# Kernel optimization log

Hardware: AMD Instinct MI355X
Metric: run time of the kernel (lower is better)

Reference implementation:

```python
import jax, jax.numpy as jnp
import numpy as np

N, T, V, C, H = 16, 512, 33, 3, 64
EPS = 1e-5
CONNECTIONS = [(0,1),(1,2),(2,3),(3,7),(0,4),(4,5),(5,6),(6,8),(9,10),(11,12),(11,13),(13,15),(12,14),(14,16),(15,17),(15,19),(15,21),(17,19),(16,18),(16,20),(16,22),(18,20),(11,23),(12,24),(23,24),(23,25),(25,27),(24,26),(26,28),(27,29),(27,31),(29,31),(28,30),(28,32)]


def _adjacency():
    A = np.zeros((V, V), dtype=np.float32)
    for i, j in CONNECTIONS:
        A[i, j] = 1.0
        A[j, i] = 1.0
    A = A + np.eye(V, dtype=np.float32)
    return jnp.asarray(A / A.sum(axis=1, keepdims=True))  # D^{-1} A row-normalization


def setup_inputs() -> dict:
    key = jax.random.key(0)
    ks = iter(jax.random.split(key, 80))
    def nrm(shape, s=0.05):
        return jax.random.normal(next(ks), shape, jnp.float32) * s
    d = {"x": jax.random.normal(next(ks), (N, T, V, C), jnp.float32), "A": _adjacency()}
    def bn(prefix, shape):
        d[prefix + "g"] = 1.0 + nrm(shape, 0.1)
        d[prefix + "b"] = nrm(shape, 0.1)
        d[prefix + "m"] = jnp.zeros(shape, jnp.float32)
        d[prefix + "v"] = jnp.ones(shape, jnp.float32)
    bn("dbn_", (C * V,))
    d["b1_gw"] = nrm((H, C)); d["b1_gb"] = nrm((H,))
    bn("b1_bn1", (H,)); d["b1_tw"] = nrm((H, H, 9)); d["b1_tb"] = nrm((H,)); bn("b1_bn2", (H,))
    d["m_gw"] = nrm((3, H, H)); d["m_gb"] = nrm((3, H))
    bn("m_bn1", (3, H)); d["m_tw"] = nrm((3, H, H, 9)); d["m_tb"] = nrm((3, H)); bn("m_bn2", (3, H))
    d["b5_gw"] = nrm((C, H)); d["b5_gb"] = nrm((C,))
    bn("b5_bn1", (C,)); d["b5_tw"] = nrm((C, C, 9)); d["b5_tb"] = nrm((C,)); bn("b5_bn2", (C,))
    return d


def _bn2d(y, g, b, m, v):
    sh = (1, -1, 1, 1)
    return (y - m.reshape(sh)) * (g.reshape(sh) * jax.lax.rsqrt(v.reshape(sh) + EPS)) + b.reshape(sh)


def _block(y, A, gw, gb, g1, b1, m1, v1, tw, tb, g2, b2, m2, v2, residual):
    res = y if residual else 0.0
    # GraphConv: 1x1 conv (K=1 partition) then joint aggregation with normalized adjacency
    z = jnp.einsum('nctv,oc->notv', y, gw) + gb.reshape(1, -1, 1, 1)
    z = jnp.einsum('nctv,vw->nctw', z, A)
    # TCN: BN -> ReLU -> 9x1 temporal conv (pad 4) -> BN (dropout identity in eval)
    z = jax.nn.relu(_bn2d(z, g1, b1, m1, v1))
    z = jax.lax.conv_general_dilated(z, tw[..., None], (1, 1), [(4, 4), (0, 0)],
                                     dimension_numbers=('NCHW', 'OIHW', 'NCHW')) + tb.reshape(1, -1, 1, 1)
    z = _bn2d(z, g2, b2, m2, v2)
    return jax.nn.relu(z + res)


def _forward(x, A, dbn_g, dbn_b, dbn_m, dbn_v, b1_gw, b1_gb, b1_bn1g, b1_bn1b, b1_bn1m, b1_bn1v, b1_tw, b1_tb, b1_bn2g, b1_bn2b, b1_bn2m, b1_bn2v, m_gw, m_gb, m_bn1g, m_bn1b, m_bn1m, m_bn1v, m_tw, m_tb, m_bn2g, m_bn2b, m_bn2m, m_bn2v, b5_gw, b5_gb, b5_bn1g, b5_bn1b, b5_bn1m, b5_bn1v, b5_tw, b5_tb, b5_bn2g, b5_bn2b, b5_bn2m, b5_bn2v):
    xc = jnp.transpose(x, (0, 3, 1, 2))  # N,C,T,V
    # data_bn: raw view of NCTV contiguous buffer as (N, C*V, T), matching torch .view
    xr = xc.reshape(N, C * V, T)
    xr = (xr - dbn_m[:, None]) * (dbn_g[:, None] * jax.lax.rsqrt(dbn_v[:, None] + EPS)) + dbn_b[:, None]
    y = xr.reshape(N, C, T, V)
    y = _block(y, A, b1_gw, b1_gb, b1_bn1g, b1_bn1b, b1_bn1m, b1_bn1v, b1_tw, b1_tb, b1_bn2g, b1_bn2b, b1_bn2m, b1_bn2v, False)
    for i in range(3):
        y = _block(y, A, m_gw[i], m_gb[i], m_bn1g[i], m_bn1b[i], m_bn1m[i], m_bn1v[i], m_tw[i], m_tb[i], m_bn2g[i], m_bn2b[i], m_bn2m[i], m_bn2v[i], True)
    y = _block(y, A, b5_gw, b5_gb, b5_bn1g, b5_bn1b, b5_bn1m, b5_bn1v, b5_tw, b5_tb, b5_bn2g, b5_bn2b, b5_bn2m, b5_bn2v, False)
    return jnp.transpose(xc + y, (0, 2, 3, 1))  # N,T,V,C


def reference(x, A, dbn_g, dbn_b, dbn_m, dbn_v, b1_gw, b1_gb, b1_bn1g, b1_bn1b, b1_bn1m, b1_bn1v, b1_tw, b1_tb, b1_bn2g, b1_bn2b, b1_bn2m, b1_bn2v, m_gw, m_gb, m_bn1g, m_bn1b, m_bn1m, m_bn1v, m_tw, m_tb, m_bn2g, m_bn2b, m_bn2m, m_bn2v, b5_gw, b5_gb, b5_bn1g, b5_bn1b, b5_bn1m, b5_bn1v, b5_tw, b5_tb, b5_bn2g, b5_bn2b, b5_bn2m, b5_bn2v):
    return _forward(x, A, dbn_g, dbn_b, dbn_m, dbn_v, b1_gw, b1_gb, b1_bn1g, b1_bn1b, b1_bn1m, b1_bn1v, b1_tw, b1_tb, b1_bn2g, b1_bn2b, b1_bn2m, b1_bn2v, m_gw, m_gb, m_bn1g, m_bn1b, m_bn1m, m_bn1v, m_tw, m_tb, m_bn2g, m_bn2b, m_bn2m, m_bn2v, b5_gw, b5_gb, b5_bn1g, b5_bn1b, b5_bn1m, b5_bn1v, b5_tw, b5_tb, b5_bn2g, b5_bn2b, b5_bn2m, b5_bn2v)
```

## Files before the change

### kernel.cpp

```cpp
#include <hip/hip_runtime.h>
#include <hip/hip_bf16.h>


constexpr int N_ = 16, T_ = 512, V_ = 33, C_ = 3, H_ = 64;
constexpr float EPS_ = 1e-5f;

typedef __attribute__((ext_vector_type(8))) short short8;
typedef __attribute__((ext_vector_type(4))) float f32x4;

__device__ inline unsigned short f2bf(float f) {
    union { __hip_bfloat16 h; unsigned short u; } cv;
    cv.h = __float2bfloat16(f);
    return cv.u;
}
__device__ inline float bf2f(unsigned short u) {
    union { unsigned short u; __hip_bfloat16 h; } cv;
    cv.u = u;
    return __bfloat162float(cv.h);
}

__global__ __launch_bounds__(256) void k_prep(
    const float* __restrict__ b1_tw, const float* __restrict__ m_tw,
    const float* __restrict__ b1_gw, const float* __restrict__ m_gw,
    const float* __restrict__ Adj,
    unsigned short* __restrict__ wT_bf, unsigned short* __restrict__ gw_bf,
    unsigned short* __restrict__ ATbf, float* __restrict__ colsum,
    float* __restrict__ gwT_b1)
{
    int idx = blockIdx.x * 256 + threadIdx.x;
    if (idx < 147456) {
        int s = idx / 36864, r = idx % 36864;
        int k = r / 4096, o = (r % 4096) / 64, i = r % 64;
        const float* src = (s == 0) ? b1_tw : (m_tw + (size_t)(s - 1) * 36864);
        wT_bf[idx] = f2bf(src[(o * 64 + i) * 9 + k]);
    } else if (idx < 147456 + 12288) {
        int r = idx - 147456;
        gw_bf[r] = f2bf(m_gw[r]);
    } else if (idx < 147456 + 12288 + 3456) {
        int r = idx - 159744;
        int w = r / 72, vv = r % 72;
        ATbf[r] = (w < 33 && vv < 33) ? f2bf(Adj[vv * 33 + w]) : (unsigned short)0;
    } else if (idx < 147456 + 12288 + 3456 + 48) {
        int w = idx - 163200;
        float s = 0.f;
        if (w < 33)
            for (int vv = 0; vv < 33; ++vv) s += Adj[vv * 33 + w];
        colsum[w] = s;
    } else if (idx < 147456 + 12288 + 3456 + 48 + 192) {
        int r = idx - 163248;
        int c = r / 64, o = r % 64;
        gwT_b1[r] = b1_gw[o * 3 + c];
    }
}

__global__ __launch_bounds__(256) void k_stageA_b1(
    const float* __restrict__ x,
    unsigned short* __restrict__ out,
    const unsigned short* __restrict__ ATbf,
    const float* __restrict__ colsum,
    const float* __restrict__ gwT,
    const float* __restrict__ gb,
    const float* __restrict__ g1, const float* __restrict__ b1,
    const float* __restrict__ m1, const float* __restrict__ v1,
    const float* __restrict__ dg, const float* __restrict__ db,
    const float* __restrict__ dm, const float* __restrict__ dv)
{
    __shared__ float sy[4][V_ * 4];
    __shared__ unsigned short UT[64 * 72];
    __shared__ float cs[48];

    int nt0 = blockIdx.x * 4;
    int tid = threadIdx.x;
    int wv = tid >> 6, lane = tid & 63;
    int l15 = lane & 15, lg = lane >> 4;
    int o = wv * 16 + l15;

    short8 atf[3][2];
#pragma unroll
    for (int mf = 0; mf < 3; ++mf)
#pragma unroll
        for (int kk = 0; kk < 2; ++kk)
            atf[mf][kk] = *reinterpret_cast<const short8*>(
                ATbf + (16 * mf + l15) * 72 + kk * 32 + lg * 8);

    float gw0 = gwT[0 * 64 + o], gw1 = gwT[1 * 64 + o], gw2 = gwT[2 * 64 + o];
    float gbl = gb[o];
    float s1 = g1[o] * rsqrtf(v1[o] + EPS_);
    float c1 = b1[o] - m1[o] * s1;

    for (int idx = tid; idx < 4 * V_ * 3; idx += 256) {
        int j = idx / (V_ * 3), r = idx % (V_ * 3);
        int v = r / 3, c = r % 3;
        int nt = nt0 + j;
        int t = nt & (T_ - 1);
        int jj = c * V_ + ((t * V_ + v) >> 9);
        float s = dg[jj] * rsqrtf(dv[jj] + EPS_);
        sy[j][v * 4 + c] = (x[(size_t)nt * (V_ * 3) + r] - dm[jj]) * s + db[jj];
    }
    for (int idx = tid; idx < 128; idx += 256) {
        int oo = idx >> 1, cc = idx & 1;
        short8 z = {};
        *reinterpret_cast<short8*>(&UT[oo * 72 + 48 + cc * 8]) = z;
    }
    if (tid < 48) cs[tid] = colsum[tid];
    __syncthreads();

    for (int j = 0; j < 4; ++j) {
#pragma unroll
        for (int it = 0; it < 12; ++it) {
            int v = lg + it * 4;
            float u = 0.f;
            if (v < V_) {
                u = sy[j][v * 4 + 0] * gw0;
                u = fmaf(sy[j][v * 4 + 1], gw1, u);
                u = fmaf(sy[j][v * 4 + 2], gw2, u);
            }
            UT[o * 72 + v] = f2bf(u);
        }
        short8 bu[2];
#pragma unroll
        for (int kk = 0; kk < 2; ++kk)
            bu[kk] = *reinterpret_cast<const short8*>(&UT[o * 72 + kk * 32 + lg * 8]);
#pragma unroll
        for (int mf2 = 0; mf2 < 3; ++mf2) {
            f32x4 az = {};
#pragma unroll
            for (int kk = 0; kk < 2; ++kk)
                az = __builtin_amdgcn_mfma_f32_16x16x32_bf16(atf[mf2][kk], bu[kk], az, 0, 0, 0);
#pragma unroll
            for (int r = 0; r < 4; ++r) {
                int w = 16 * mf2 + lg * 4 + r;
                if (w < 33) {
                    float val = az[r] + gbl * cs[w];
                    float y = fmaxf(val * s1 + c1, 0.f);
                    out[((size_t)(nt0 + j) * V_ + w) * 64 + o] = f2bf(y);
                }
            }
        }
    }
}

__global__ __launch_bounds__(256) void k_stageA_mfma(
    const unsigned short* __restrict__ in,
    unsigned short* __restrict__ out,
    const unsigned short* __restrict__ ATbf,
    const float* __restrict__ colsum,
    const unsigned short* __restrict__ gwbf,
    const float* __restrict__ gb,
    const float* __restrict__ g1, const float* __restrict__ b1,
    const float* __restrict__ m1, const float* __restrict__ v1)
{
    __shared__ unsigned short Ys[4 * 48 * 72];
    __shared__ unsigned short UT[64 * 72];
    __shared__ float cs[48];

    int nt0 = blockIdx.x * 4;
    int tid = threadIdx.x;
    int wv = tid >> 6, lane = tid & 63;
    int l15 = lane & 15, lg = lane >> 4;
    int o = wv * 16 + l15;

    short8 atf[3][2];
#pragma unroll
    for (int mf = 0; mf < 3; ++mf)
#pragma unroll
        for (int kk = 0; kk < 2; ++kk)
            atf[mf][kk] = *reinterpret_cast<const short8*>(
                ATbf + (16 * mf + l15) * 72 + kk * 32 + lg * 8);
    short8 gwf[2];
#pragma unroll
    for (int kk = 0; kk < 2; ++kk)
        gwf[kk] = *reinterpret_cast<const short8*>(gwbf + o * 64 + kk * 32 + lg * 8);

    float gbl = gb[o];
    float s1 = g1[o] * rsqrtf(v1[o] + EPS_);
    float c1 = b1[o] - m1[o] * s1;

    for (int idx = tid; idx < 1056; idx += 256) {
        int j = idx / 264, r = idx % 264;
        int v = r >> 3, cc = r & 7;
        *reinterpret_cast<short8*>(&Ys[(j * 48 + v) * 72 + cc * 8]) =
            *reinterpret_cast<const short8*>(in + ((size_t)(nt0 + j) * V_ + v) * 64 + cc * 8);
    }
    for (int idx = tid; idx < 540; idx += 256) {
        int j = idx / 135, r = idx % 135;
        int v = 33 + r / 9, cc = r % 9;
        short8 z = {};
        *reinterpret_cast<short8*>(&Ys[(j * 48 + v) * 72 + cc * 8]) = z;
    }
    for (int idx = tid; idx < 128; idx += 256) {
        int oo = idx >> 1, cc = idx & 1;
        short8 z = {};
        *reinterpret_cast<short8*>(&UT[oo * 72 + 48 + cc * 8]) = z;
    }
    if (tid < 48) cs[tid] = colsum[tid];
    __syncthreads();

    for (int j = 0; j < 4; ++j) {
#pragma unroll
        for (int mf = 0; mf < 3; ++mf) {
            f32x4 au = {};
#pragma unroll
            for (int kk = 0; kk < 2; ++kk) {
                short8 a = *reinterpret_cast<const short8*>(
                    &Ys[(j * 48 + 16 * mf + l15) * 72 + kk * 32 + lg * 8]);
                au = __builtin_amdgcn_mfma_f32_16x16x32_bf16(a, gwf[kk], au, 0, 0, 0);
            }
            unsigned short pk[4];
            pk[0] = f2bf(au[0]); pk[1] = f2bf(au[1]);
            pk[2] = f2bf(au[2]); pk[3] = f2bf(au[3]);
            *reinterpret_cast<ushort4*>(&UT[o * 72 + 16 * mf + lg * 4]) =
                *reinterpret_cast<ushort4*>(pk);
        }
        short8 bu[2];
#pragma unroll
        for (int kk = 0; kk < 2; ++kk)
            bu[kk] = *reinterpret_cast<const short8*>(&UT[o * 72 + kk * 32 + lg * 8]);
#pragma unroll
        for (int mf2 = 0; mf2 < 3; ++mf2) {
            f32x4 az = {};
#pragma unroll
            for (int kk = 0; kk < 2; ++kk)
                az = __builtin_amdgcn_mfma_f32_16x16x32_bf16(atf[mf2][kk], bu[kk], az, 0, 0, 0);
#pragma unroll
            for (int r = 0; r < 4; ++r) {
                int w = 16 * mf2 + lg * 4 + r;
                if (w < 33) {
                    float val = az[r] + gbl * cs[w];
                    float y = fmaxf(val * s1 + c1, 0.f);
                    out[((size_t)(nt0 + j) * V_ + w) * 64 + o] = f2bf(y);
                }
            }
        }
    }
}

template <bool RES>
__global__ __launch_bounds__(256) void k_stageB_mfma(
    const unsigned short* __restrict__ z,
    unsigned short* __restrict__ out,
    const unsigned short* __restrict__ wbf,
    const float* __restrict__ tb,
    const float* __restrict__ g2, const float* __restrict__ b2,
    const float* __restrict__ m2, const float* __restrict__ vv2)
{
    __shared__ unsigned short sa[2][72 * 64];

    int bx = blockIdx.x, v = blockIdx.y, n = blockIdx.z;
    int base_t0 = bx * 256;
    int tid = threadIdx.x;
    int wv = tid >> 6, lane = tid & 63;
    int l15 = lane & 15, lg = lane >> 4;
    int o = wv * 16 + l15;

    short8 bw[18];
#pragma unroll
    for (int k = 0; k < 9; ++k)
#pragma unroll
        for (int c = 0; c < 2; ++c)
            bw[k * 2 + c] = *reinterpret_cast<const short8*>(
                wbf + ((k * 64 + o) * 64) + c * 32 + lg * 8);

    float s2 = g2[o] * rsqrtf(vv2[o] + EPS_);
    float c2 = (tb[o] - m2[o]) * s2 + b2[o];

    short8 stg[3];

#define LOADJ(jj)                                                             \
    {                                                                         \
        int t0l = base_t0 + (jj) * 64;                                        \
        _Pragma("unroll")                                                     \
        for (int it = 0; it < 3; ++it) {                                      \
            int idx = tid + it * 256;                                         \
            if (idx < 576) {                                                  \
                int r = idx >> 3;                                             \
                int tg = t0l - 4 + r;                                         \
                short8 val = {};                                              \
                if (tg >= 0 && tg < T_)                                       \
                    val = *reinterpret_cast<const short8*>(                   \
                        z + ((size_t)(n * T_ + tg) * V_ + v) * 64 +           \
                        (idx & 7) * 8);                                       \
                stg[it] = val;                                                \
            }                                                                 \
        }                                                                     \
    }

#define WRITEJ(pp)                                                            \
    {                                                                         \
        _Pragma("unroll")                                                     \
        for (int it = 0; it < 3; ++it) {                                      \
            int idx = tid + it * 256;                                         \
            if (idx < 576) {                                                  \
                int r = idx >> 3, cc = idx & 7;                               \
                int slot = cc ^ (r & 7);                                      \
                *reinterpret_cast<short8*>(                                   \
                    reinterpret_cast<char*>(&sa[pp][0]) + r * 128 +           \
                    slot * 16) = stg[it];                                     \
            }                                                                 \
        }                                                                     \
    }

    LOADJ(0);
    WRITEJ(0);
    __syncthreads();

    int p = 0;
    for (int j = 0; j < 4; ++j) {
        if (j < 3) LOADJ(j + 1);

        int t0 = base_t0 + j * 64;

        unsigned short res[16];
        if (RES) {
#pragma unroll
            for (int f = 0; f < 4; ++f)
#pragma unroll
                for (int r = 0; r < 4; ++r) {
                    int t = t0 + f * 16 + lg * 4 + r;
                    res[f * 4 + r] =
                        out[((size_t)(n * T_ + t) * V_ + v) * 64 + o];
                }
        }

        f32x4 acc[4] = {};
        for (int k = 0; k < 9; ++k) {
#pragma unroll
            for (int c = 0; c < 2; ++c) {
                short8 b = bw[k * 2 + c];
#pragma unroll
                for (int f = 0; f < 4; ++f) {
                    int r = f * 16 + l15 + k;
                    int slot = (c * 4 + lg) ^ (r & 7);
                    short8 a = *reinterpret_cast<const short8*>(
                        reinterpret_cast<const char*>(&sa[p][0]) + r * 128 + slot * 16);
                    acc[f] = __builtin_amdgcn_mfma_f32_16x16x32_bf16(a, b, acc[f], 0, 0, 0);
                }
            }
        }

#pragma unroll
        for (int f = 0; f < 4; ++f) {
#pragma unroll
            for (int r = 0; r < 4; ++r) {
                int t = t0 + f * 16 + lg * 4 + r;
                size_t addr = ((size_t)(n * T_ + t) * V_ + v) * 64 + o;
                float zz = acc[f][r] * s2 + c2;
                if (RES) zz += bf2f(res[f * 4 + r]);
                out[addr] = f2bf(fmaxf(zz, 0.f));
            }
        }

        if (j < 3) WRITEJ(p ^ 1);
        __syncthreads();
        p ^= 1;
    }
#undef LOADJ
#undef WRITEJ
}

__global__ __launch_bounds__(256) void k_stageA_b5(
    const unsigned short* __restrict__ in,
    float* __restrict__ out,
    const float* __restrict__ Adj,
    const float* __restrict__ gw,
    const float* __restrict__ gb,
    const float* __restrict__ g1, const float* __restrict__ b1,
    const float* __restrict__ m1, const float* __restrict__ v1)
{
    __shared__ float sy[V_ * 64];
    __shared__ float su[V_ * 4];
    __shared__ float sA[V_ * V_];
    int nt = blockIdx.x;
    int tid = threadIdx.x;
    const unsigned short* src = in + (size_t)nt * (V_ * 64);
    for (int idx = tid; idx < 264; idx += 256) {
        short8 val = *reinterpret_cast<const short8*>(src + idx * 8);
#pragma unroll
        for (int e = 0; e < 8; ++e)
            sy[idx * 8 + e] = bf2f((unsigned short)val[e]);
    }
    for (int idx = tid; idx < V_ * V_; idx += 256) sA[idx] = Adj[idx];
    __syncthreads();
    for (int idx = tid; idx < V_ * 3; idx += 256) {
        int v = idx / 3, o = idx % 3;
        float a = gb[o];
        for (int c = 0; c < 64; ++c) a = fmaf(sy[v * 64 + c], gw[o * 64 + c], a);
        su[v * 4 + o] = a;
    }
    __syncthreads();
    for (int idx = tid; idx < V_ * 3; idx += 256) {
        int w = idx / 3, o = idx % 3;
        float a = 0.f;
        for (int vv = 0; vv < V_; ++vv) a = fmaf(su[vv * 4 + o], sA[vv * V_ + w], a);
        float s = g1[o] * rsqrtf(v1[o] + EPS_);
        float zz = (a - m1[o]) * s + b1[o];
        out[(size_t)nt * (V_ * 3) + w * 3 + o] = fmaxf(zz, 0.f);
    }
}

__global__ __launch_bounds__(256) void k_stageB_b5(
    const float* __restrict__ z5,
    const float* __restrict__ x,
    float* __restrict__ out,
    const float* __restrict__ tw,
    const float* __restrict__ tb,
    const float* __restrict__ g2, const float* __restrict__ b2,
    const float* __restrict__ m2, const float* __restrict__ v2)
{
    int idx = blockIdx.x * 256 + threadIdx.x;
    if (idx >= N_ * T_ * V_) return;
    int v = idx % V_;
    int t = (idx / V_) % T_;
    int n = idx / (V_ * T_);
    float acc0 = tb[0], acc1 = tb[1], acc2 = tb[2];
    for (int k = 0; k < 9; ++k) {
        int tg = t + k - 4;
        if (tg < 0 || tg >= T_) continue;
        const float* zp = &z5[((size_t)(n * T_ + tg) * V_ + v) * 3];
        float zi0 = zp[0], zi1 = zp[1], zi2 = zp[2];
        acc0 = fmaf(tw[0 * 9 + k], zi0, acc0);
        acc0 = fmaf(tw[1 * 9 + k], zi1, acc0);
        acc0 = fmaf(tw[2 * 9 + k], zi2, acc0);
        acc1 = fmaf(tw[3 * 9 + k], zi0, acc1);
        acc1 = fmaf(tw[4 * 9 + k], zi1, acc1);
        acc1 = fmaf(tw[5 * 9 + k], zi2, acc1);
        acc2 = fmaf(tw[6 * 9 + k], zi0, acc2);
        acc2 = fmaf(tw[7 * 9 + k], zi1, acc2);
        acc2 = fmaf(tw[8 * 9 + k], zi2, acc2);
    }
    size_t base = (size_t)idx * 3;
    float a[3] = {acc0, acc1, acc2};
#pragma unroll
    for (int oo = 0; oo < 3; ++oo) {
        float s = g2[oo] * rsqrtf(v2[oo] + EPS_);
        float zz = (a[oo] - m2[oo]) * s + b2[oo];
        out[base + oo] = x[base + oo] + fmaxf(zz, 0.f);
    }
}

extern "C" void kernel_launch(void* const* d_in, const int* in_sizes, int n_in,
                              void* d_out, int out_size, void* d_ws, size_t ws_size,
                              hipStream_t stream) {
    int a = 0;
    const float* x      = (const float*)d_in[a++];
    const float* Adj    = (const float*)d_in[a++];
    const float* dbn_g  = (const float*)d_in[a++];
    const float* dbn_b  = (const float*)d_in[a++];
    const float* dbn_m  = (const float*)d_in[a++];
    const float* dbn_v  = (const float*)d_in[a++];
    const float* b1_gw  = (const float*)d_in[a++];
    const float* b1_gb  = (const float*)d_in[a++];
    const float* b1_bn1g = (const float*)d_in[a++];
    const float* b1_bn1b = (const float*)d_in[a++];
    const float* b1_bn1m = (const float*)d_in[a++];
    const float* b1_bn1v = (const float*)d_in[a++];
    const float* b1_tw  = (const float*)d_in[a++];
    const float* b1_tb  = (const float*)d_in[a++];
    const float* b1_bn2g = (const float*)d_in[a++];
    const float* b1_bn2b = (const float*)d_in[a++];
    const float* b1_bn2m = (const float*)d_in[a++];
    const float* b1_bn2v = (const float*)d_in[a++];
    const float* m_gw   = (const float*)d_in[a++];
    const float* m_gb   = (const float*)d_in[a++];
    const float* m_bn1g = (const float*)d_in[a++];
    const float* m_bn1b = (const float*)d_in[a++];
    const float* m_bn1m = (const float*)d_in[a++];
    const float* m_bn1v = (const float*)d_in[a++];
    const float* m_tw   = (const float*)d_in[a++];
    const float* m_tb   = (const float*)d_in[a++];
    const float* m_bn2g = (const float*)d_in[a++];
    const float* m_bn2b = (const float*)d_in[a++];
    const float* m_bn2m = (const float*)d_in[a++];
    const float* m_bn2v = (const float*)d_in[a++];
    const float* b5_gw  = (const float*)d_in[a++];
    const float* b5_gb  = (const float*)d_in[a++];
    const float* b5_bn1g = (const float*)d_in[a++];
    const float* b5_bn1b = (const float*)d_in[a++];
    const float* b5_bn1m = (const float*)d_in[a++];
    const float* b5_bn1v = (const float*)d_in[a++];
    const float* b5_tw  = (const float*)d_in[a++];
    const float* b5_tb  = (const float*)d_in[a++];
    const float* b5_bn2g = (const float*)d_in[a++];
    const float* b5_bn2b = (const float*)d_in[a++];
    const float* b5_bn2m = (const float*)d_in[a++];
    const float* b5_bn2v = (const float*)d_in[a++];

    char* ws = (char*)d_ws;
    const size_t S_BIG_B  = (size_t)N_ * T_ * V_ * 64 * 2;
    const size_t S_SM_B   = (size_t)N_ * T_ * V_ * 3 * 4;
    unsigned short* B0     = (unsigned short*)(ws);
    unsigned short* B1     = (unsigned short*)(ws + S_BIG_B);
    float*          z5     = (float*)(ws + 2 * S_BIG_B + S_SM_B);
    unsigned short* wT_bf  = (unsigned short*)(ws + 2 * S_BIG_B + 2 * S_SM_B);
    unsigned short* gw_bf  = wT_bf + 147456;
    unsigned short* ATbf   = gw_bf + 12288;
    float*          colsum = (float*)(ATbf + 3456);
    float*          gwT_b1 = colsum + 48;

    k_prep<<<(163440 + 255) / 256, 256, 0, stream>>>(
        b1_tw, m_tw, b1_gw, m_gw, Adj, wT_bf, gw_bf, ATbf, colsum, gwT_b1);

    k_stageA_b1<<<(N_ * T_) / 4, 256, 0, stream>>>(
        x, B1, ATbf, colsum, gwT_b1, b1_gb, b1_bn1g, b1_bn1b, b1_bn1m, b1_bn1v,
        dbn_g, dbn_b, dbn_m, dbn_v);
    k_stageB_mfma<false><<<dim3(T_ / 256, V_, N_), 256, 0, stream>>>(
        B1, B0, wT_bf, b1_tb, b1_bn2g, b1_bn2b, b1_bn2m, b1_bn2v);

    for (int i = 0; i < 3; ++i) {
        k_stageA_mfma<<<(N_ * T_) / 4, 256, 0, stream>>>(
            B0, B1, ATbf, colsum, gw_bf + i * 4096, m_gb + i * 64,
            m_bn1g + i * 64, m_bn1b + i * 64, m_bn1m + i * 64, m_bn1v + i * 64);
        k_stageB_mfma<true><<<dim3(T_ / 256, V_, N_), 256, 0, stream>>>(
            B1, B0, wT_bf + (1 + i) * 36864, m_tb + i * 64,
            m_bn2g + i * 64, m_bn2b + i * 64, m_bn2m + i * 64, m_bn2v + i * 64);
    }

    k_stageA_b5<<<N_ * T_, 256, 0, stream>>>(
        B0, z5, Adj, b5_gw, b5_gb, b5_bn1g, b5_bn1b, b5_bn1m, b5_bn1v);
    k_stageB_b5<<<(N_ * T_ * V_ + 255) / 256, 256, 0, stream>>>(
        z5, x, (float*)d_out, b5_tw, b5_tb, b5_bn2g, b5_bn2b, b5_bn2m, b5_bn2v);
}
```

Baseline: 270.3 us.

## Rewrite final-block graph conv with bf16 MFMA, four timesteps per block

The last block's graph convolution (64->3 channel projection plus adjacency aggregation) now runs on bf16 MFMA instructions, using a zero-padded 16x64 weight prepared in the prep kernel and the existing transposed adjacency. Each workgroup handles four (n,t) slices, one per wavefront, instead of one slice per block with scalar FMA loops. The bias is folded in through the adjacency column sums. This cuts the scalar ALU work and the block count for this stage, at the cost of bf16 rounding of the intermediate projection and wasted MFMA lanes, since only 3 of 16 output rows are used.

After: 254.3 us. -5.9%, faster.

```diff
diff --git a/kernel.cpp b/kernel.cpp
--- a/kernel.cpp
+++ b/kernel.cpp
@@ -22,10 +22,11 @@
 __global__ __launch_bounds__(256) void k_prep(
     const float* __restrict__ b1_tw, const float* __restrict__ m_tw,
     const float* __restrict__ b1_gw, const float* __restrict__ m_gw,
+    const float* __restrict__ b5_gw,
     const float* __restrict__ Adj,
     unsigned short* __restrict__ wT_bf, unsigned short* __restrict__ gw_bf,
     unsigned short* __restrict__ ATbf, float* __restrict__ colsum,
-    float* __restrict__ gwT_b1)
+    float* __restrict__ gwT_b1, unsigned short* __restrict__ gwpad_b5)
 {
     int idx = blockIdx.x * 256 + threadIdx.x;
     if (idx < 147456) {
@@ -50,6 +51,10 @@
         int r = idx - 163248;
         int c = r / 64, o = r % 64;
         gwT_b1[r] = b1_gw[o * 3 + c];
+    } else if (idx < 147456 + 12288 + 3456 + 48 + 192 + 1024) {
+        int r = idx - 163440;
+        int o16 = r / 64, c = r % 64;
+        gwpad_b5[r] = (o16 < 3) ? f2bf(b5_gw[o16 * 64 + c]) : (unsigned short)0;
     }
 }
 
@@ -361,40 +366,97 @@
 __global__ __launch_bounds__(256) void k_stageA_b5(
     const unsigned short* __restrict__ in,
     float* __restrict__ out,
-    const float* __restrict__ Adj,
-    const float* __restrict__ gw,
+    const unsigned short* __restrict__ ATbf,
+    const float* __restrict__ colsum,
+    const unsigned short* __restrict__ gwpad,
     const float* __restrict__ gb,
     const float* __restrict__ g1, const float* __restrict__ b1,
     const float* __restrict__ m1, const float* __restrict__ v1)
 {
-    __shared__ float sy[V_ * 64];
-    __shared__ float su[V_ * 4];
-    __shared__ float sA[V_ * V_];
-    int nt = blockIdx.x;
+    __shared__ unsigned short Ys[4 * 48 * 72];
+    __shared__ unsigned short UT[64 * 72];
+    __shared__ float cs[48];
+
+    int nt0 = blockIdx.x * 4;
     int tid = threadIdx.x;
-    const unsigned short* src = in + (size_t)nt * (V_ * 64);
-    for (int idx = tid; idx < 264; idx += 256) {
-        short8 val = *reinterpret_cast<const short8*>(src + idx * 8);
-#pragma unroll
-        for (int e = 0; e < 8; ++e)
-            sy[idx * 8 + e] = bf2f((unsigned short)val[e]);
-    }
-    for (int idx = tid; idx < V_ * V_; idx += 256) sA[idx] = Adj[idx];
+    int wv = tid >> 6, lane = tid & 63;
+    int l15 = lane & 15, lg = lane >> 4;
+    int urow = wv * 16 + l15;
+
+    short8 atf[3][2];
+#pragma unroll
+    for (int mf = 0; mf < 3; ++mf)
+#pragma unroll
+        for (int kk = 0; kk < 2; ++kk)
+            atf[mf][kk] = *reinterpret_cast<const short8*>(
+                ATbf + (16 * mf + l15) * 72 + kk * 32 + lg * 8);
+    short8 gwf[2];
+#pragma unroll
+    for (int kk = 0; kk < 2; ++kk)
+        gwf[kk] = *reinterpret_cast<const short8*>(gwpad + l15 * 64 + kk * 32 + lg * 8);
+
+    float gbl = 0.f, s1 = 0.f, c1 = 0.f;
+    if (l15 < 3) {
+        gbl = gb[l15];
+        s1 = g1[l15] * rsqrtf(v1[l15] + EPS_);
+        c1 = b1[l15] - m1[l15] * s1;
+    }
+
+    for (int idx = tid; idx < 1056; idx += 256) {
+        int j = idx / 264, r = idx % 264;
+        int v = r >> 3, cc = r & 7;
+        *reinterpret_cast<short8*>(&Ys[(j * 48 + v) * 72 + cc * 8]) =
+            *reinterpret_cast<const short8*>(in + ((size_t)(nt0 + j) * V_ + v) * 64 + cc * 8);
+    }
+    for (int idx = tid; idx < 540; idx += 256) {
+        int j = idx / 135, r = idx % 135;
+        int v = 33 + r / 9, cc = r % 9;
+        short8 z = {};
+        *reinterpret_cast<short8*>(&Ys[(j * 48 + v) * 72 + cc * 8]) = z;
+    }
+    for (int idx = tid; idx < 128; idx += 256) {
+        int oo = idx >> 1, cc = idx & 1;
+        short8 z = {};
+        *reinterpret_cast<short8*>(&UT[oo * 72 + 48 + cc * 8]) = z;
+    }
+    if (tid < 48) cs[tid] = colsum[tid];
     __syncthreads();
-    for (int idx = tid; idx < V_ * 3; idx += 256) {
-        int v = idx / 3, o = idx % 3;
-        float a = gb[o];
-        for (int c = 0; c < 64; ++c) a = fmaf(sy[v * 64 + c], gw[o * 64 + c], a);
-        su[v * 4 + o] = a;
-    }
-    __syncthreads();
-    for (int idx = tid; idx < V_ * 3; idx += 256) {
-        int w = idx / 3, o = idx % 3;
-        float a = 0.f;
-        for (int vv = 0; vv < V_; ++vv) a = fmaf(su[vv * 4 + o], sA[vv * V_ + w], a);
-        float s = g1[o] * rsqrtf(v1[o] + EPS_);
-        float zz = (a - m1[o]) * s + b1[o];
-        out[(size_t)nt * (V_ * 3) + w * 3 + o] = fmaxf(zz, 0.f);
+
+    int j = wv;
+#pragma unroll
+    for (int mf = 0; mf < 3; ++mf) {
+        f32x4 au = {};
+#pragma unroll
+        for (int kk = 0; kk < 2; ++kk) {
+            short8 a = *reinterpret_cast<const short8*>(
+                &Ys[(j * 48 + 16 * mf + l15) * 72 + kk * 32 + lg * 8]);
+            au = __builtin_amdgcn_mfma_f32_16x16x32_bf16(a, gwf[kk], au, 0, 0, 0);
+        }
+        unsigned short pk[4];
+        pk[0] = f2bf(au[0]); pk[1] = f2bf(au[1]);
+        pk[2] = f2bf(au[2]); pk[3] = f2bf(au[3]);
+        *reinterpret_cast<ushort4*>(&UT[urow * 72 + 16 * mf + lg * 4]) =
+            *reinterpret_cast<ushort4*>(pk);
+    }
+    short8 bu[2];
+#pragma unroll
+    for (int kk = 0; kk < 2; ++kk)
+        bu[kk] = *reinterpret_cast<const short8*>(&UT[urow * 72 + kk * 32 + lg * 8]);
+#pragma unroll
+    for (int mf2 = 0; mf2 < 3; ++mf2) {
+        f32x4 az = {};
+#pragma unroll
+        for (int kk = 0; kk < 2; ++kk)
+            az = __builtin_amdgcn_mfma_f32_16x16x32_bf16(atf[mf2][kk], bu[kk], az, 0, 0, 0);
+#pragma unroll
+        for (int r = 0; r < 4; ++r) {
+            int w = 16 * mf2 + lg * 4 + r;
+            if (w < 33 && l15 < 3) {
+                float val = az[r] + gbl * cs[w];
+                float y = fmaxf(val * s1 + c1, 0.f);
+                out[(size_t)(nt0 + j) * (V_ * 3) + w * 3 + l15] = y;
+            }
+        }
     }
 }
 
@@ -496,9 +558,11 @@
     unsigned short* ATbf   = gw_bf + 12288;
     float*          colsum = (float*)(ATbf + 3456);
     float*          gwT_b1 = colsum + 48;
-
-    k_prep<<<(163440 + 255) / 256, 256, 0, stream>>>(
-        b1_tw, m_tw, b1_gw, m_gw, Adj, wT_bf, gw_bf, ATbf, colsum, gwT_b1);
+    unsigned short* gwpad_b5 = (unsigned short*)(gwT_b1 + 192);
+
+    k_prep<<<(164464 + 255) / 256, 256, 0, stream>>>(
+        b1_tw, m_tw, b1_gw, m_gw, b5_gw, Adj,
+        wT_bf, gw_bf, ATbf, colsum, gwT_b1, gwpad_b5);
 
     k_stageA_b1<<<(N_ * T_) / 4, 256, 0, stream>>>(
         x, B1, ATbf, colsum, gwT_b1, b1_gb, b1_bn1g, b1_bn1b, b1_bn1m, b1_bn1v,
@@ -515,8 +579,9 @@
             m_bn2g + i * 64, m_bn2b + i * 64, m_bn2m + i * 64, m_bn2v + i * 64);
     }
 
-    k_stageA_b5<<<N_ * T_, 256, 0, stream>>>(
-        B0, z5, Adj, b5_gw, b5_gb, b5_bn1g, b5_bn1b, b5_bn1m, b5_bn1v);
+    k_stageA_b5<<<(N_ * T_) / 4, 256, 0, stream>>>(
+        B0, z5, ATbf, colsum, gwpad_b5, b5_gb,
+        b5_bn1g, b5_bn1b, b5_bn1m, b5_bn1v);
     k_stageB_b5<<<(N_ * T_ * V_ + 255) / 256, 256, 0, stream>>>(
         z5, x, (float*)d_out, b5_tw, b5_tb, b5_bn2g, b5_bn2b, b5_bn2m, b5_bn2v);
 }
```
